# Optimization experiments

Measured on AMD Instinct MI355X. Metric: run time of the kernel, lower is better.

The kernel has to match this reference:

```python
import jax, jax.numpy as jnp
import numpy as np

D_MODEL, N_HEAD, D_FF = 768, 12, 3072
HEAD_DIM = D_MODEL // N_HEAD
EPS = 1e-5


def _layernorm(x, g, b):
    mu = jnp.mean(x, axis=-1, keepdims=True)
    var = jnp.mean((x - mu) ** 2, axis=-1, keepdims=True)
    return (x - mu) * jax.lax.rsqrt(var + EPS) * g + b


def setup_inputs() -> dict:
    key = jax.random.key(0)
    ks = jax.random.split(key, 14)
    s = 1.0 / np.sqrt(D_MODEL)
    sf = 1.0 / np.sqrt(D_FF)
    inp = {
        "x": jax.random.normal(ks[0], (2, 2048, D_MODEL), dtype=jnp.float32),
        "Wq": jax.random.normal(ks[1], (D_MODEL, D_MODEL), dtype=jnp.float32) * s,
        "bq": jnp.zeros((D_MODEL,), jnp.float32),
        "Wk": jax.random.normal(ks[2], (D_MODEL, D_MODEL), dtype=jnp.float32) * s,
        "bk": jnp.zeros((D_MODEL,), jnp.float32),
        "Wv": jax.random.normal(ks[3], (D_MODEL, D_MODEL), dtype=jnp.float32) * s,
        "bv": jnp.zeros((D_MODEL,), jnp.float32),
        "Wo": jax.random.normal(ks[4], (D_MODEL, D_MODEL), dtype=jnp.float32) * s,
        "bo": jnp.zeros((D_MODEL,), jnp.float32),
        "W1": jax.random.normal(ks[5], (D_MODEL, D_FF), dtype=jnp.float32) * s,
        "b1": jnp.zeros((D_FF,), jnp.float32),
        "W2": jax.random.normal(ks[6], (D_FF, D_MODEL), dtype=jnp.float32) * sf,
        "b2": jnp.zeros((D_MODEL,), jnp.float32),
        "ln1_g": jnp.ones((D_MODEL,), jnp.float32),
        "ln1_b": jnp.zeros((D_MODEL,), jnp.float32),
        "ln2_g": jnp.ones((D_MODEL,), jnp.float32),
        "ln2_b": jnp.zeros((D_MODEL,), jnp.float32),
    }
    return inp


def reference(x, Wq, bq, Wk, bk, Wv, bv, Wo, bo, W1, b1, W2, b2,
              ln1_g, ln1_b, ln2_g, ln2_b):
    B, S, D = x.shape
    # projections -> [B, H, S, hd]
    def proj(W, b):
        return (x @ W + b).reshape(B, S, N_HEAD, HEAD_DIM).transpose(0, 2, 1, 3)
    q, k, v = proj(Wq, bq), proj(Wk, bk), proj(Wv, bv)
    scores = jnp.einsum("bhqd,bhkd->bhqk", q, k) / jnp.sqrt(
        jnp.asarray(HEAD_DIM, jnp.float32))
    attn = jax.nn.softmax(scores, axis=-1)
    ctx = jnp.einsum("bhqk,bhkd->bhqd", attn, v)
    ctx = ctx.transpose(0, 2, 1, 3).reshape(B, S, D)
    attn_out = ctx @ Wo + bo
    h = _layernorm(x + attn_out, ln1_g, ln1_b)
    ffn = jax.nn.gelu(h @ W1 + b1, approximate=False) @ W2 + b2
    return _layernorm(h + ffn, ln2_g, ln2_b)
```

## Files before the change

kernel.cpp:

```cpp
#include <hip/hip_runtime.h>
#include <hip/hip_bf16.h>
#include <cstdint>
#include <cstddef>

typedef unsigned short u16;
typedef __bf16 bf16x8 __attribute__((ext_vector_type(8)));
typedef float f32x4 __attribute__((ext_vector_type(4)));

#define MFMA_BF16(a, b, c) __builtin_amdgcn_mfma_f32_16x16x32_bf16((a), (b), (c), 0, 0, 0)

#define GLDS16(g, l)                                                        \
  __builtin_amdgcn_global_load_lds(                                         \
      (__attribute__((address_space(1))) void*)(void*)(g),                  \
      (__attribute__((address_space(3))) void*)(void*)(l), 16, 0, 0)

#define QSCALE 0.18033688011112042f
#define PSTRIDE ((size_t)4096 * 768)

__device__ __forceinline__ u16 f2bf(float x) {
  union { float f; unsigned u; } c; c.f = x;
  unsigned u = c.u;
  unsigned r = (u + 0x7fffu + ((u >> 16) & 1u)) >> 16;
  return (u16)r;
}


__global__ __launch_bounds__(256) void transpose_bf16_k(
    const float* __restrict__ in, u16* __restrict__ out, int K, int N) {
  __shared__ float tile[32][33];
  const int tx = threadIdx.x & 31, ty = threadIdx.x >> 5;
  const int bx = blockIdx.x * 32;
  const int by = blockIdx.y * 32;
#pragma unroll
  for (int j = 0; j < 32; j += 8)
    tile[ty + j][tx] = in[(size_t)(by + ty + j) * N + bx + tx];
  __syncthreads();
#pragma unroll
  for (int j = 0; j < 32; j += 8)
    out[(size_t)(bx + ty + j) * K + by + tx] = f2bf(tile[tx][ty + j]);
}

__global__ __launch_bounds__(256) void cvt_bf16_k(
    const float* __restrict__ in, u16* __restrict__ out, int n) {
  int i = (blockIdx.x * 256 + threadIdx.x) * 4;
  if (i + 3 < n) {
    const float4 v = *(const float4*)(in + i);
    ushort4 o;
    o.x = f2bf(v.x); o.y = f2bf(v.y); o.z = f2bf(v.z); o.w = f2bf(v.w);
    *(ushort4*)(out + i) = o;
  }
}

__global__ __launch_bounds__(256) void concat3_k(
    const float* __restrict__ a, const float* __restrict__ b,
    const float* __restrict__ c, float* __restrict__ out) {
  int i = blockIdx.x * 256 + threadIdx.x;
  if (i < 768) out[i] = a[i];
  else if (i < 1536) out[i] = b[i - 768];
  else if (i < 2304) out[i] = c[i - 1536];
}

template <int EPI>
__global__ __launch_bounds__(256) void gemm_bt(
    const u16* __restrict__ A, const u16* __restrict__ BT,
    const float* __restrict__ bias, int M, int N, int K, int kchunk,
    float* __restrict__ outf, u16* __restrict__ outb,
    u16* __restrict__ qo, u16* __restrict__ ko, u16* __restrict__ vto) {
  __shared__ __align__(16) u16 lsA[128 * 64];
  __shared__ __align__(16) u16 lsB[128 * 64];
  const int tid = threadIdx.x;
  const int w = tid >> 6, lane = tid & 63;
  const int wm = w & 1, wn = w >> 1;
  const int lrow = lane & 15, quad = lane >> 4;
  const int m0 = blockIdx.y * 128, n0 = blockIdx.x * 128;
  const int kbeg = blockIdx.z * kchunk, kend = kbeg + kchunk;

  f32x4 acc[4][4];
#pragma unroll
  for (int i = 0; i < 4; ++i)
#pragma unroll
    for (int j = 0; j < 4; ++j) acc[i][j] = (f32x4){0.f, 0.f, 0.f, 0.f};

  const int off = tid * 16;
  const int srow = off >> 7;
  const int schunk = (off >> 4) & 7;
  const int sxc = schunk ^ (srow & 7);
  const int scol = sxc * 8;

  const int rsw = lrow & 7;

  for (int k0 = kbeg; k0 < kend; k0 += 64) {
    const u16* ga = A + (size_t)(m0 + srow) * K + k0 + scol;
    const u16* gb = BT + (size_t)(n0 + srow) * K + k0 + scol;
#pragma unroll
    for (int c = 0; c < 4; ++c) {
      GLDS16(ga + (size_t)(c * 32) * K, (char*)lsA + c * 4096 + off);
      GLDS16(gb + (size_t)(c * 32) * K, (char*)lsB + c * 4096 + off);
    }
    __syncthreads();
#pragma unroll
    for (int ks = 0; ks < 2; ++ks) {
      const int slot = ((ks * 4 + quad) ^ rsw) * 8;
      bf16x8 af[4], bfr[4];
#pragma unroll
      for (int ms = 0; ms < 4; ++ms)
        af[ms] = *(const bf16x8*)&lsA[(wm * 64 + ms * 16 + lrow) * 64 + slot];
#pragma unroll
      for (int ns = 0; ns < 4; ++ns)
        bfr[ns] = *(const bf16x8*)&lsB[(wn * 64 + ns * 16 + lrow) * 64 + slot];
#pragma unroll
      for (int ms = 0; ms < 4; ++ms)
#pragma unroll
        for (int ns = 0; ns < 4; ++ns)
          acc[ms][ns] = MFMA_BF16(af[ms], bfr[ns], acc[ms][ns]);
    }
    __syncthreads();
  }

  float* const pf = (EPI == 3) ? outf + (size_t)blockIdx.z * M * N : outf;
#pragma unroll
  for (int ms = 0; ms < 4; ++ms) {
    const int rbase = m0 + wm * 64 + ms * 16 + quad * 4;
#pragma unroll
    for (int ns = 0; ns < 4; ++ns) {
      const int col = n0 + wn * 64 + ns * 16 + lrow;
      if constexpr (EPI == 3) {
#pragma unroll
        for (int r = 0; r < 4; ++r)
          pf[(size_t)(rbase + r) * N + col] = acc[ms][ns][r];
      } else if constexpr (EPI == 2) {
        const float bcol = bias[col];
#pragma unroll
        for (int r = 0; r < 4; ++r) {
          float v = acc[ms][ns][r] + bcol;
          float g = 0.5f * v * (1.0f + erff(v * 0.7071067811865476f));
          outb[(size_t)(rbase + r) * N + col] = f2bf(g);
        }
      } else {
        const float bcol = bias[col];
        const int which = col / 768;
        const int rem = col - which * 768;
        const int hh = rem >> 6, dd = rem & 63;
        const int bI = rbase >> 11, sI = rbase & 2047;
        const size_t bh = (size_t)bI * 12 + hh;
        if (which == 0) {
#pragma unroll
          for (int r = 0; r < 4; ++r)
            qo[(bh * 2048 + sI + r) * 64 + dd] = f2bf((acc[ms][ns][r] + bcol) * QSCALE);
        } else if (which == 1) {
#pragma unroll
          for (int r = 0; r < 4; ++r)
            ko[(bh * 2048 + sI + r) * 64 + dd] = f2bf(acc[ms][ns][r] + bcol);
        } else {
          ushort4 pk;
          pk.x = f2bf(acc[ms][ns][0] + bcol);
          pk.y = f2bf(acc[ms][ns][1] + bcol);
          pk.z = f2bf(acc[ms][ns][2] + bcol);
          pk.w = f2bf(acc[ms][ns][3] + bcol);
          *(ushort4*)(vto + (bh * 64 + dd) * 2048 + sI) = pk;
        }
      }
    }
  }
}

__global__ __launch_bounds__(256) void attn_kernel(
    const u16* __restrict__ q, const u16* __restrict__ k,
    const u16* __restrict__ vT, u16* __restrict__ opart,
    float* __restrict__ lpart) {
  __shared__ __align__(16) u16 lsK[2 * 64 * 64];
  __shared__ __align__(16) u16 lsV[2 * 64 * 64];
  __shared__ __align__(16) u16 lsP[4][32 * 64];
  const int tid = threadIdx.x;
  const int w = tid >> 6, lane = tid & 63;
  const int lrow = lane & 15, quad = lane >> 4;
  const int bh = blockIdx.y;
  const int b = bh / 12, h = bh - b * 12;
  const int q0 = blockIdx.x * 128;
  const int z = blockIdx.z;
  const int kvbeg = z * 1024;

  const u16* qbase = q + (size_t)bh * 2048 * 64;
  const u16* kbase = k + (size_t)bh * 2048 * 64;
  const u16* vbase = vT + (size_t)bh * 64 * 2048;

  bf16x8 qf[2][2];
#pragma unroll
  for (int m = 0; m < 2; ++m) {
    const int qrow = q0 + w * 32 + m * 16 + lrow;
    qf[m][0] = *(const bf16x8*)(qbase + (size_t)qrow * 64 + quad * 8);
    qf[m][1] = *(const bf16x8*)(qbase + (size_t)qrow * 64 + 32 + quad * 8);
  }

  float lsum[2][4] = {{0.f, 0.f, 0.f, 0.f}, {0.f, 0.f, 0.f, 0.f}};
  f32x4 oacc[2][4];
#pragma unroll
  for (int m = 0; m < 2; ++m)
#pragma unroll
    for (int d = 0; d < 4; ++d) oacc[m][d] = (f32x4){0.f, 0.f, 0.f, 0.f};

  const int off = tid * 16;
  const int srow = off >> 7;
  const int schunk = (off >> 4) & 7;
  const int sxc = schunk ^ (srow & 7);
  const int ksrc = srow * 64 + sxc * 8;
  const int vsrc0 = srow * 2048 + sxc * 8;

  const int c0 = quad ^ (lrow & 7);
  const int rd0 = c0 * 8, rd1 = (c0 ^ 4) * 8;

  u16* const lsPw = &lsP[w][0];
  const int jhi_base = lrow >> 3, jlo = lrow & 7;

  auto stage = [&](int kt, int buf) {
    char* dk = (char*)(lsK + buf * 4096);
    char* dv = (char*)(lsV + buf * 4096);
    GLDS16(kbase + (size_t)kt * 64 + ksrc, dk + off);
    GLDS16(kbase + (size_t)(kt + 32) * 64 + ksrc, dk + 4096 + off);
    GLDS16(vbase + vsrc0 + kt, dv + off);
    GLDS16(vbase + vsrc0 + kt + 32 * 2048, dv + 4096 + off);
  };

  stage(kvbeg, 0);
  for (int t = 0; t < 16; ++t) {
    __syncthreads();
    if (t < 15) stage(kvbeg + (t + 1) * 64, (t + 1) & 1);
    const u16* Kb = lsK + (t & 1) * 4096;
    const u16* Vb = lsV + (t & 1) * 4096;

    f32x4 sc[2][4];
#pragma unroll
    for (int ns = 0; ns < 4; ++ns) {
      const u16* kr = Kb + (ns * 16 + lrow) * 64;
      bf16x8 kf0 = *(const bf16x8*)(kr + rd0);
      bf16x8 kf1 = *(const bf16x8*)(kr + rd1);
#pragma unroll
      for (int m = 0; m < 2; ++m) {
        sc[m][ns] = (f32x4){0.f, 0.f, 0.f, 0.f};
        sc[m][ns] = MFMA_BF16(qf[m][0], kf0, sc[m][ns]);
        sc[m][ns] = MFMA_BF16(qf[m][1], kf1, sc[m][ns]);
      }
    }

#pragma unroll
    for (int m = 0; m < 2; ++m)
#pragma unroll
      for (int ns = 0; ns < 4; ++ns) {
        const int jhi = ns * 2 + jhi_base;
#pragma unroll
        for (int r = 0; r < 4; ++r) {
          float p = __builtin_amdgcn_exp2f(sc[m][ns][r]);
          lsum[m][r] += p;
          union { float f; unsigned u; } cv; cv.f = p;
          const int row7 = (quad * 4 + r) & 7;
          lsPw[(m * 16 + quad * 4 + r) * 64 + ((jhi ^ row7) * 8) + jlo] =
              (u16)(cv.u >> 16);
        }
      }

#pragma unroll
    for (int d = 0; d < 4; ++d) {
      const u16* vr = Vb + (d * 16 + lrow) * 64;
      bf16x8 vf0 = *(const bf16x8*)(vr + rd0);
      bf16x8 vf1 = *(const bf16x8*)(vr + rd1);
#pragma unroll
      for (int m = 0; m < 2; ++m) {
        const u16* pr = lsPw + (m * 16 + lrow) * 64;
        bf16x8 pf0 = *(const bf16x8*)(pr + rd0);
        bf16x8 pf1 = *(const bf16x8*)(pr + rd1);
        oacc[m][d] = MFMA_BF16(pf0, vf0, oacc[m][d]);
        oacc[m][d] = MFMA_BF16(pf1, vf1, oacc[m][d]);
      }
    }
  }

#pragma unroll
  for (int m = 0; m < 2; ++m)
#pragma unroll
    for (int r = 0; r < 4; ++r) {
#pragma unroll
      for (int mm = 1; mm <= 8; mm <<= 1)
        lsum[m][r] += __shfl_xor(lsum[m][r], mm);
    }

  u16* const op = opart + (size_t)z * PSTRIDE;
#pragma unroll
  for (int m = 0; m < 2; ++m) {
    const int srow_out = q0 + w * 32 + m * 16 + quad * 4;
#pragma unroll
    for (int d = 0; d < 4; ++d)
#pragma unroll
      for (int r = 0; r < 4; ++r)
        op[(size_t)(b * 2048 + srow_out + r) * 768 + h * 64 + d * 16 + lrow] =
            f2bf(oacc[m][d][r]);
    if (lrow == 0) {
#pragma unroll
      for (int r = 0; r < 4; ++r)
        lpart[(size_t)(z * 24 + bh) * 2048 + srow_out + r] = lsum[m][r];
    }
  }
}

__global__ __launch_bounds__(256) void attn_combine_k(
    const u16* __restrict__ op, const float* __restrict__ lp,
    u16* __restrict__ ctx) {
  const unsigned idx = (blockIdx.x * 256u + threadIdx.x) * 4u;
  const unsigned row = idx / 768u;
  const unsigned c = idx - row * 768u;
  const int b = row >> 11, s = row & 2047;
  const int h = c >> 6;
  const size_t li = (size_t)(b * 12 + h) * 2048 + s;
  const float rinv = 1.f / (lp[li] + lp[(size_t)24 * 2048 + li]);
  ushort4 o0 = *(const ushort4*)(op + idx);
  ushort4 o1 = *(const ushort4*)(op + PSTRIDE + idx);
  ushort4 out;
  union { unsigned u; float f; } a, bb2;
#define CMB(fld) \
  a.u = (unsigned)o0.fld << 16; bb2.u = (unsigned)o1.fld << 16; \
  out.fld = f2bf((a.f + bb2.f) * rinv);
  CMB(x) CMB(y) CMB(z) CMB(w)
#undef CMB
  *(ushort4*)(ctx + idx) = out;
}

__global__ __launch_bounds__(256) void ln_kernel(
    const float* __restrict__ parts, int nparts, const float* __restrict__ bias,
    const float* __restrict__ res, const float* __restrict__ g,
    const float* __restrict__ bb, float* __restrict__ outf, u16* __restrict__ outb) {
  const int row = blockIdx.x;
  const int tid = threadIdx.x;
  const float* pr = res + (size_t)row * 768;
  float v[3], s = 0.f, s2 = 0.f;
#pragma unroll
  for (int j = 0; j < 3; ++j) {
    const int c = tid + j * 256;
    float t = bias[c] + pr[c];
    for (int p = 0; p < nparts; ++p)
      t += parts[p * PSTRIDE + (size_t)row * 768 + c];
    v[j] = t; s += t; s2 += t * t;
  }
#pragma unroll
  for (int m = 32; m > 0; m >>= 1) {
    s += __shfl_xor(s, m);
    s2 += __shfl_xor(s2, m);
  }
  __shared__ float red[8];
  const int w = tid >> 6, lane = tid & 63;
  if (lane == 0) { red[w] = s; red[4 + w] = s2; }
  __syncthreads();
  s = red[0] + red[1] + red[2] + red[3];
  s2 = red[4] + red[5] + red[6] + red[7];
  const float mu = s * (1.f / 768.f);
  const float var = s2 * (1.f / 768.f) - mu * mu;
  const float rstd = rsqrtf(var + 1e-5f);
#pragma unroll
  for (int j = 0; j < 3; ++j) {
    const int c = tid + j * 256;
    const float y = (v[j] - mu) * rstd * g[c] + bb[c];
    if (outf) outf[(size_t)row * 768 + c] = y;
    if (outb) outb[(size_t)row * 768 + c] = f2bf(y);
  }
}

extern "C" void kernel_launch(void* const* d_in, const int* in_sizes, int n_in,
                              void* d_out, int out_size, void* d_ws, size_t ws_size,
                              hipStream_t stream) {
  const float* x    = (const float*)d_in[0];
  const float* Wq   = (const float*)d_in[1];
  const float* bq   = (const float*)d_in[2];
  const float* Wk   = (const float*)d_in[3];
  const float* bk   = (const float*)d_in[4];
  const float* Wv   = (const float*)d_in[5];
  const float* bv   = (const float*)d_in[6];
  const float* Wo   = (const float*)d_in[7];
  const float* bo   = (const float*)d_in[8];
  const float* W1   = (const float*)d_in[9];
  const float* b1   = (const float*)d_in[10];
  const float* W2   = (const float*)d_in[11];
  const float* b2   = (const float*)d_in[12];
  const float* ln1g = (const float*)d_in[13];
  const float* ln1b = (const float*)d_in[14];
  const float* ln2g = (const float*)d_in[15];
  const float* ln2b = (const float*)d_in[16];

  char* ws = (char*)d_ws;
  size_t off = 0;
  auto alloc = [&](size_t bytes) {
    void* p = ws + off;
    off += (bytes + 255) & ~(size_t)255;
    return p;
  };
  u16*  WqkvT = (u16*)alloc(2304ull * 768 * 2);
  u16*  WoT   = (u16*)alloc(768ull * 768 * 2);
  u16*  W1T   = (u16*)alloc(3072ull * 768 * 2);
  u16*  W2T   = (u16*)alloc(768ull * 3072 * 2);
  float* bqkv = (float*)alloc(2304 * 4);
  char* bigbase = (char*)alloc(0);
  u16*  xb    = (u16*)alloc(4096ull * 768 * 2);
  u16*  qb    = (u16*)alloc(24ull * 2048 * 64 * 2);
  u16*  kb    = (u16*)alloc(24ull * 2048 * 64 * 2);
  u16*  vtb   = (u16*)alloc(24ull * 64 * 2048 * 2);
  u16*  ctx   = (u16*)alloc(4096ull * 768 * 2);
  float* attno = (float*)alloc(2ull * PSTRIDE * 4);
  float* f2b   = (float*)bigbase;
  u16*   opart = (u16*)attno;
  float* lpart = (float*)((char*)attno + 2 * PSTRIDE * 2);
  float* hbuf  = (float*)alloc(4096ull * 768 * 4);
  u16*  hb    = (u16*)alloc(4096ull * 768 * 2);
  u16*  f1    = (u16*)alloc(4096ull * 3072 * 2);

  transpose_bf16_k<<<dim3(24, 24), 256, 0, stream>>>(Wq, WqkvT, 768, 768);
  transpose_bf16_k<<<dim3(24, 24), 256, 0, stream>>>(Wk, WqkvT + 768 * 768, 768, 768);
  transpose_bf16_k<<<dim3(24, 24), 256, 0, stream>>>(Wv, WqkvT + 2 * 768 * 768, 768, 768);
  transpose_bf16_k<<<dim3(24, 24), 256, 0, stream>>>(Wo, WoT, 768, 768);
  transpose_bf16_k<<<dim3(96, 24), 256, 0, stream>>>(W1, W1T, 768, 3072);
  transpose_bf16_k<<<dim3(24, 96), 256, 0, stream>>>(W2, W2T, 3072, 768);
  concat3_k<<<9, 256, 0, stream>>>(bq, bk, bv, bqkv);
  cvt_bf16_k<<<3072, 256, 0, stream>>>(x, xb, 4096 * 768);

  gemm_bt<0><<<dim3(18, 32, 1), 256, 0, stream>>>(xb, WqkvT, bqkv, 4096, 2304, 768, 768,
                                                  nullptr, nullptr, qb, kb, vtb);
  attn_kernel<<<dim3(16, 24, 2), 256, 0, stream>>>(qb, kb, vtb, opart, lpart);
  attn_combine_k<<<3072, 256, 0, stream>>>(opart, lpart, ctx);
  gemm_bt<3><<<dim3(6, 32, 2), 256, 0, stream>>>(ctx, WoT, nullptr, 4096, 768, 768, 384,
                                                 attno, nullptr, nullptr, nullptr, nullptr);
  ln_kernel<<<4096, 256, 0, stream>>>(attno, 2, bo, x, ln1g, ln1b, hbuf, hb);
  gemm_bt<2><<<dim3(24, 32, 1), 256, 0, stream>>>(hb, W1T, b1, 4096, 3072, 768, 768,
                                                  nullptr, f1, nullptr, nullptr, nullptr);
  gemm_bt<3><<<dim3(6, 32, 4), 256, 0, stream>>>(f1, W2T, nullptr, 4096, 768, 3072, 768,
                                                 f2b, nullptr, nullptr, nullptr, nullptr);
  ln_kernel<<<4096, 256, 0, stream>>>(f2b, 4, b2, hbuf, ln2g, ln2b, (float*)d_out, nullptr);
}
```

Baseline: 317.7 us.

## Double-buffer GEMM LDS tiles with BK=32 and merge four weight transposes

```diff
diff --git a/kernel.cpp b/kernel.cpp
--- a/kernel.cpp
+++ b/kernel.cpp
@@ -25,12 +25,35 @@
 }
 
 
+__global__ __launch_bounds__(256) void transpose4_k(
+    const float* __restrict__ s0, const float* __restrict__ s1,
+    const float* __restrict__ s2, const float* __restrict__ s3,
+    u16* __restrict__ d0, u16* __restrict__ d1,
+    u16* __restrict__ d2, u16* __restrict__ d3) {
+  __shared__ float tile[32][33];
+  const float* in; u16* out;
+  switch (blockIdx.z) {
+    case 0: in = s0; out = d0; break;
+    case 1: in = s1; out = d1; break;
+    case 2: in = s2; out = d2; break;
+    default: in = s3; out = d3; break;
+  }
+  const int tx = threadIdx.x & 31, ty = threadIdx.x >> 5;
+  const int bx = blockIdx.x * 32, by = blockIdx.y * 32;
+#pragma unroll
+  for (int j = 0; j < 32; j += 8)
+    tile[ty + j][tx] = in[(size_t)(by + ty + j) * 768 + bx + tx];
+  __syncthreads();
+#pragma unroll
+  for (int j = 0; j < 32; j += 8)
+    out[(size_t)(bx + ty + j) * 768 + by + tx] = f2bf(tile[tx][ty + j]);
+}
+
 __global__ __launch_bounds__(256) void transpose_bf16_k(
     const float* __restrict__ in, u16* __restrict__ out, int K, int N) {
   __shared__ float tile[32][33];
   const int tx = threadIdx.x & 31, ty = threadIdx.x >> 5;
-  const int bx = blockIdx.x * 32;
-  const int by = blockIdx.y * 32;
+  const int bx = blockIdx.x * 32, by = blockIdx.y * 32;
 #pragma unroll
   for (int j = 0; j < 32; j += 8)
     tile[ty + j][tx] = in[(size_t)(by + ty + j) * N + bx + tx];
@@ -66,14 +89,14 @@
     const float* __restrict__ bias, int M, int N, int K, int kchunk,
     float* __restrict__ outf, u16* __restrict__ outb,
     u16* __restrict__ qo, u16* __restrict__ ko, u16* __restrict__ vto) {
-  __shared__ __align__(16) u16 lsA[128 * 64];
-  __shared__ __align__(16) u16 lsB[128 * 64];
+  __shared__ __align__(16) u16 lsA[2 * 128 * 32];
+  __shared__ __align__(16) u16 lsB[2 * 128 * 32];
   const int tid = threadIdx.x;
   const int w = tid >> 6, lane = tid & 63;
   const int wm = w & 1, wn = w >> 1;
   const int lrow = lane & 15, quad = lane >> 4;
   const int m0 = blockIdx.y * 128, n0 = blockIdx.x * 128;
-  const int kbeg = blockIdx.z * kchunk, kend = kbeg + kchunk;
+  const int kbeg = blockIdx.z * kchunk;
 
   f32x4 acc[4][4];
 #pragma unroll
@@ -82,39 +105,44 @@
     for (int j = 0; j < 4; ++j) acc[i][j] = (f32x4){0.f, 0.f, 0.f, 0.f};
 
   const int off = tid * 16;
-  const int srow = off >> 7;
-  const int schunk = (off >> 4) & 7;
-  const int sxc = schunk ^ (srow & 7);
+  const int srow = off >> 6;
+  const int schunk = (off >> 4) & 3;
+  const int sxc = schunk ^ (srow & 3);
   const int scol = sxc * 8;
 
-  const int rsw = lrow & 7;
-
-  for (int k0 = kbeg; k0 < kend; k0 += 64) {
-    const u16* ga = A + (size_t)(m0 + srow) * K + k0 + scol;
-    const u16* gb = BT + (size_t)(n0 + srow) * K + k0 + scol;
-#pragma unroll
-    for (int c = 0; c < 4; ++c) {
-      GLDS16(ga + (size_t)(c * 32) * K, (char*)lsA + c * 4096 + off);
-      GLDS16(gb + (size_t)(c * 32) * K, (char*)lsB + c * 4096 + off);
-    }
+  const u16* ga0 = A + (size_t)(m0 + srow) * K + scol;
+  const u16* gb0 = BT + (size_t)(n0 + srow) * K + scol;
+
+  auto stage = [&](int k0, int buf) {
+    char* da = (char*)(lsA + buf * 4096);
+    char* db = (char*)(lsB + buf * 4096);
+    GLDS16(ga0 + k0, da + off);
+    GLDS16(ga0 + k0 + (size_t)64 * K, da + 4096 + off);
+    GLDS16(gb0 + k0, db + off);
+    GLDS16(gb0 + k0 + (size_t)64 * K, db + 4096 + off);
+  };
+
+  const int rs = (quad ^ (lrow & 3)) * 8;
+
+  const int niter = kchunk >> 5;
+  stage(kbeg, 0);
+  for (int t = 0; t < niter; ++t) {
     __syncthreads();
-#pragma unroll
-    for (int ks = 0; ks < 2; ++ks) {
-      const int slot = ((ks * 4 + quad) ^ rsw) * 8;
-      bf16x8 af[4], bfr[4];
-#pragma unroll
-      for (int ms = 0; ms < 4; ++ms)
-        af[ms] = *(const bf16x8*)&lsA[(wm * 64 + ms * 16 + lrow) * 64 + slot];
+    if (t + 1 < niter) stage(kbeg + (t + 1) * 32, (t + 1) & 1);
+    const u16* Ab = lsA + (t & 1) * 4096;
+    const u16* Bb = lsB + (t & 1) * 4096;
+    bf16x8 af[4], bfr[4];
+#pragma unroll
+    for (int ms = 0; ms < 4; ++ms)
+      af[ms] = *(const bf16x8*)&Ab[(wm * 64 + ms * 16 + lrow) * 32 + rs];
+#pragma unroll
+    for (int ns = 0; ns < 4; ++ns)
+      bfr[ns] = *(const bf16x8*)&Bb[(wn * 64 + ns * 16 + lrow) * 32 + rs];
+#pragma unroll
+    for (int ms = 0; ms < 4; ++ms)
 #pragma unroll
       for (int ns = 0; ns < 4; ++ns)
-        bfr[ns] = *(const bf16x8*)&lsB[(wn * 64 + ns * 16 + lrow) * 64 + slot];
-#pragma unroll
-      for (int ms = 0; ms < 4; ++ms)
-#pragma unroll
-        for (int ns = 0; ns < 4; ++ns)
-          acc[ms][ns] = MFMA_BF16(af[ms], bfr[ns], acc[ms][ns]);
-    }
-    __syncthreads();
+        acc[ms][ns] = MFMA_BF16(af[ms], bfr[ns], acc[ms][ns]);
   }
 
   float* const pf = (EPI == 3) ? outf + (size_t)blockIdx.z * M * N : outf;
@@ -409,10 +437,8 @@
   u16*  hb    = (u16*)alloc(4096ull * 768 * 2);
   u16*  f1    = (u16*)alloc(4096ull * 3072 * 2);
 
-  transpose_bf16_k<<<dim3(24, 24), 256, 0, stream>>>(Wq, WqkvT, 768, 768);
-  transpose_bf16_k<<<dim3(24, 24), 256, 0, stream>>>(Wk, WqkvT + 768 * 768, 768, 768);
-  transpose_bf16_k<<<dim3(24, 24), 256, 0, stream>>>(Wv, WqkvT + 2 * 768 * 768, 768, 768);
-  transpose_bf16_k<<<dim3(24, 24), 256, 0, stream>>>(Wo, WoT, 768, 768);
+  transpose4_k<<<dim3(24, 24, 4), 256, 0, stream>>>(
+      Wq, Wk, Wv, Wo, WqkvT, WqkvT + 768 * 768, WqkvT + 2 * 768 * 768, WoT);
   transpose_bf16_k<<<dim3(96, 24), 256, 0, stream>>>(W1, W1T, 768, 3072);
   transpose_bf16_k<<<dim3(24, 96), 256, 0, stream>>>(W2, W2T, 3072, 768);
   concat3_k<<<9, 256, 0, stream>>>(bq, bk, bv, bqkv);
```

Result: faster. 311.3 us (-2.0%).
